# Performance work log

Measured on AMD Instinct MI355X. Metric: run time of the kernel, lower is better.

The kernel has to match this reference:

```python
import jax, jax.numpy as jnp
import numpy as np

B, N, D = 8, 4096, 64
NPOINT, NSAMPLE, RADIUS = 1024, 32, 0.2
MLP = [64, 64, 128]
IN_CH = 3 + D
EPS = 1e-5  # BatchNorm eps (torch default)


def setup_inputs() -> dict:
    key = jax.random.key(0)
    ks = jax.random.split(key, 2 + len(MLP))
    inp = {
        "xyz": jax.random.uniform(ks[0], (B, N, 3), jnp.float32),   # points in unit cube
        "points": jax.random.normal(ks[1], (B, N, D), jnp.float32),  # per-point features
    }
    last = IN_CH
    for i, out in enumerate(MLP):
        inp[f"w{i}"] = jax.random.normal(ks[2 + i], (out, last), jnp.float32) * 0.05  # 1x1 conv weight
        inp[f"b{i}"] = jnp.zeros((out,), jnp.float32)   # conv bias
        inp[f"g{i}"] = jnp.ones((out,), jnp.float32)    # BN gamma
        inp[f"be{i}"] = jnp.zeros((out,), jnp.float32)  # BN beta
        inp[f"m{i}"] = jnp.zeros((out,), jnp.float32)   # BN running mean
        inp[f"v{i}"] = jnp.ones((out,), jnp.float32)    # BN running var
        last = out
    return inp


def _fps(xyz, npoint):
    # Iterative farthest point sampling (deterministic start at index 0).
    Bb, Nn, _ = xyz.shape
    def step(carry, _):
        dist, far = carry
        centroid = xyz[jnp.arange(Bb), far][:, None, :]            # [B,1,3]
        d = jnp.sum((xyz - centroid) ** 2, axis=-1)                # [B,N]
        dist = jnp.minimum(dist, d)
        nfar = jnp.argmax(dist, axis=-1).astype(jnp.int32)
        return (dist, nfar), far
    init = (jnp.full((Bb, Nn), 1e10, xyz.dtype), jnp.zeros((Bb,), jnp.int32))
    _, idx = jax.lax.scan(step, init, None, length=npoint)
    return idx.T                                                   # [B,npoint]


def _index(p, idx):
    # p: [B,N,C], idx: [B,...] -> [B,...,C]
    return jax.vmap(lambda a, i: a[i])(p, idx)


def _ball_query(xyz, new_xyz):
    # For each query center, take first NSAMPLE point indices within RADIUS,
    # padding with the first found index (exactly PointNet++ query_ball_point).
    Nn = xyz.shape[1]
    sqr = jnp.sum((new_xyz[:, :, None, :] - xyz[:, None, :, :]) ** 2, axis=-1)  # [B,S,N]
    gidx = jnp.where(sqr > RADIUS ** 2, Nn, jnp.arange(Nn)[None, None, :])
    gidx = jnp.sort(gidx, axis=-1)[:, :, :NSAMPLE]                 # [B,S,K]
    first = gidx[:, :, :1]
    return jnp.where(gidx == Nn, first, gidx)


def reference(xyz, points, w0, b0, g0, be0, m0, v0,
              w1, b1, g1, be1, m1, v1,
              w2, b2, g2, be2, m2, v2):
    fps_idx = _fps(xyz, NPOINT)
    new_xyz = _index(xyz, fps_idx)                                 # [B,S,3]
    gidx = _ball_query(xyz, new_xyz)                               # [B,S,K]
    grouped_xyz = _index(xyz, gidx) - new_xyz[:, :, None, :]       # local coords [B,S,K,3]
    grouped_pts = _index(points, gidx)                             # [B,S,K,D]
    x = jnp.concatenate([grouped_xyz, grouped_pts], axis=-1)       # [B,S,K,3+D]
    layers = ((w0, b0, g0, be0, m0, v0),
              (w1, b1, g1, be1, m1, v1),
              (w2, b2, g2, be2, m2, v2))
    for w, b, g, be, m, v in layers:
        x = jnp.einsum('bskc,oc->bsko', x, w) + b                  # 1x1 conv (pointwise MLP)
        x = g * (x - m) * jax.lax.rsqrt(v + EPS) + be              # BN (eval mode)
        x = jax.nn.relu(x)
    new_points = jnp.max(x, axis=2)                                # max over neighbors -> [B,S,Cout]
    return new_xyz, new_points
```

## Files before the change

### kernel.cpp

```cpp
#include <hip/hip_runtime.h>
#include <hip/hip_bf16.h>
#include <stdint.h>

#define BATCH   8
#define NPTS    4096
#define DCH     64
#define NPOINT  1024
#define NSAMPLE 32
#define NEWXYZ_FLOATS (BATCH * NPOINT * 3)

typedef float v2f __attribute__((ext_vector_type(2)));

__device__ __forceinline__ float sqdist_rn(float px, float py, float pz,
                                           float cx, float cy, float cz) {
    float dx = __fsub_rn(px, cx);
    float dy = __fsub_rn(py, cy);
    float dz = __fsub_rn(pz, cz);
    return __fadd_rn(__fadd_rn(__fmul_rn(dx, dx), __fmul_rn(dy, dy)), __fmul_rn(dz, dz));
}

__device__ __forceinline__ unsigned long long ullmax(unsigned long long a, unsigned long long b) {
    return a > b ? a : b;
}

template <int CTRL>
__device__ __forceinline__ unsigned long long dpp_u64(unsigned long long v) {
    int lo = (int)(unsigned)(v & 0xFFFFFFFFull);
    int hi = (int)(unsigned)(v >> 32);
    lo = __builtin_amdgcn_update_dpp(0, lo, CTRL, 0xF, 0xF, true);
    hi = __builtin_amdgcn_update_dpp(0, hi, CTRL, 0xF, 0xF, true);
    return ((unsigned long long)(unsigned)hi << 32) | (unsigned)lo;
}

__global__ void prep_kernel(const float* __restrict__ w0, const float* __restrict__ b0,
                            const float* __restrict__ g0, const float* __restrict__ be0,
                            const float* __restrict__ m0, const float* __restrict__ v0,
                            const float* __restrict__ w1, const float* __restrict__ b1,
                            const float* __restrict__ g1, const float* __restrict__ be1,
                            const float* __restrict__ m1, const float* __restrict__ v1,
                            const float* __restrict__ w2, const float* __restrict__ b2,
                            const float* __restrict__ g2, const float* __restrict__ be2,
                            const float* __restrict__ m2, const float* __restrict__ v2,
                            float* __restrict__ wT0, float* __restrict__ wT1,
                            float* __restrict__ wT2, float* __restrict__ st) {
    const int tid  = blockIdx.x * blockDim.x + threadIdx.x;
    const int nthr = gridDim.x * blockDim.x;
    for (int i = tid; i < 64 * 67; i += nthr) {
        int o = i / 67, c = i % 67;
        wT0[c * 64 + (((o & 7) << 3) | (o >> 3))] = w0[i];
    }
    for (int i = tid; i < 64 * 64; i += nthr) {
        int o = i >> 6, c = i & 63;
        wT1[c * 64 + (((o & 7) << 3) | (o >> 3))] = w1[i];
    }
    for (int i = tid; i < 128 * 64; i += nthr) { int o = i >> 6, c = i & 63; wT2[c * 128 + o] = w2[i]; }
    if (tid < 64) {
        const int col = ((tid & 7) << 3) | (tid >> 3);
        float s = g0[tid] / sqrtf(v0[tid] + 1e-5f);
        st[col] = s;
        st[64 + col] = (b0[tid] - m0[tid]) * s + be0[tid];
        s = g1[tid] / sqrtf(v1[tid] + 1e-5f);
        st[128 + col] = s;
        st[192 + col] = (b1[tid] - m1[tid]) * s + be1[tid];
    }
    if (tid < 128) {
        float s = g2[tid] / sqrtf(v2[tid] + 1e-5f);
        st[256 + tid] = s;
        st[384 + tid] = (b2[tid] - m2[tid]) * s + be2[tid];
    }
}

__global__ __launch_bounds__(512, 1) void fps_kernel(const float* __restrict__ xyz,
                                                     float* __restrict__ newxyz) {
    __shared__ float4 sxyz[NPTS];
    __shared__ float4 snew[NPOINT];
    __shared__ unsigned long long kbuf[3];
    const int b    = blockIdx.x;
    const int tid  = threadIdx.x;
    const int lane = tid & 63;
    const float* xb = xyz + (size_t)b * NPTS * 3;

    v2f px[4], py[4], pz[4];
    float dd[8];
    unsigned invj[8];
#pragma unroll
    for (int i = 0; i < 8; ++i) {
        const int j = tid + i * 512;
        const float x = xb[3 * j], y = xb[3 * j + 1], z = xb[3 * j + 2];
        sxyz[j] = make_float4(x, y, z, 0.f);
        px[i >> 1][i & 1] = x;
        py[i >> 1][i & 1] = y;
        pz[i >> 1][i & 1] = z;
        dd[i] = 1e10f;
        invj[i] = 0xFFFFFFFFu - (unsigned)j;
    }
    if (tid < 3) kbuf[tid] = 0ull;

    float cx = xb[0], cy = xb[1], cz = xb[2];
    if (tid == 0) snew[0] = make_float4(cx, cy, cz, 0.f);
    __syncthreads();

    for (int t = 1; t < NPOINT; ++t) {
        const v2f ncx = {-cx, -cx}, ncy = {-cy, -cy}, ncz = {-cz, -cz};
#pragma unroll
        for (int k = 0; k < 4; ++k) {
            v2f dx, dy, dz, qx, qy, qz, s1, s2;
            asm("v_pk_add_f32 %0, %1, %2" : "=v"(dx) : "v"(px[k]), "v"(ncx));
            asm("v_pk_add_f32 %0, %1, %2" : "=v"(dy) : "v"(py[k]), "v"(ncy));
            asm("v_pk_add_f32 %0, %1, %2" : "=v"(dz) : "v"(pz[k]), "v"(ncz));
            asm("v_pk_mul_f32 %0, %1, %1" : "=v"(qx) : "v"(dx));
            asm("v_pk_mul_f32 %0, %1, %1" : "=v"(qy) : "v"(dy));
            asm("v_pk_mul_f32 %0, %1, %1" : "=v"(qz) : "v"(dz));
            asm("v_pk_add_f32 %0, %1, %2" : "=v"(s1) : "v"(qx), "v"(qy));
            asm("v_pk_add_f32 %0, %1, %2" : "=v"(s2) : "v"(s1), "v"(qz));
            dd[2 * k]     = fminf(dd[2 * k],     s2[0]);
            dd[2 * k + 1] = fminf(dd[2 * k + 1], s2[1]);
        }
        const float m = fmaxf(fmaxf(fmaxf(dd[0], dd[1]), fmaxf(dd[2], dd[3])),
                              fmaxf(fmaxf(dd[4], dd[5]), fmaxf(dd[6], dd[7])));
        unsigned inv = invj[0];
#pragma unroll
        for (int i = 7; i >= 0; --i)
            if (dd[i] == m) inv = invj[i];
        unsigned long long key =
            ((unsigned long long)__float_as_uint(m) << 32) | (unsigned long long)inv;
        key = ullmax(key, dpp_u64<0x111>(key));
        key = ullmax(key, dpp_u64<0x112>(key));
        key = ullmax(key, dpp_u64<0x114>(key));
        key = ullmax(key, dpp_u64<0x118>(key));
        key = ullmax(key, dpp_u64<0x142>(key));
        key = ullmax(key, dpp_u64<0x143>(key));
        if (lane == 63) atomicMax(&kbuf[t % 3], key);
        if (tid == 0) kbuf[(t + 1) % 3] = 0ull;
        __syncthreads();

        const unsigned long long v = kbuf[t % 3];
        const unsigned widx = 0xFFFFFFFFu - (unsigned)(v & 0xFFFFFFFFull);
        const float4 c = sxyz[widx];
        cx = c.x; cy = c.y; cz = c.z;
        if (tid == 0) snew[t] = make_float4(cx, cy, cz, 0.f);
    }
    __syncthreads();

    float* ob = newxyz + (size_t)b * NPOINT * 3;
    const float* sn = (const float*)snew;
#pragma unroll
    for (int k = tid; k < NPOINT * 3; k += 512) {
        const int p = k / 3, c = k - 3 * p;
        ob[k] = sn[4 * p + c];
    }
}

__global__ __launch_bounds__(256) void ballq_kernel(const float* __restrict__ xyz,
                                                    const float* __restrict__ newxyz,
                                                    int* __restrict__ gidx) {
    __shared__ int g[4][NSAMPLE];
    const int lane = threadIdx.x & 63;
    const int w    = threadIdx.x >> 6;
    const int q    = blockIdx.x * 4 + w;
    const int b    = q >> 10;
    const float* xb = xyz + (size_t)b * NPTS * 3;
    const float* c  = newxyz + (size_t)q * 3;
    const float cx = c[0], cy = c[1], cz = c[2];
    const float r2 = 0.04f;

    int cnt = 0;
    for (int base = 0; base < NPTS; base += 64) {
        const int j = base + lane;
        const float d = sqdist_rn(xb[j * 3 + 0], xb[j * 3 + 1], xb[j * 3 + 2], cx, cy, cz);
        const bool keep = !(d > r2);
        const unsigned long long m = __ballot(keep);
        if (keep) {
            const int slot = cnt + __popcll(m & ((1ull << lane) - 1ull));
            if (slot < NSAMPLE) g[w][slot] = j;
        }
        cnt += (int)__popcll(m);
        if (cnt >= NSAMPLE) break;
    }
    __syncthreads();
    const int first = g[w][0];
    if (lane < NSAMPLE) {
        const int v = (lane < cnt) ? g[w][lane] : first;
        gidx[(size_t)q * NSAMPLE + lane] = v;
    }
}

__global__ __launch_bounds__(256) void mlp_kernel(
    const float* __restrict__ xyz, const float* __restrict__ points,
    const float* __restrict__ newxyz, const int* __restrict__ gidx,
    const float* __restrict__ wT0, const float* __restrict__ wT1,
    const float* __restrict__ wT2, const float* __restrict__ st,
    float* __restrict__ outp) {
    __shared__ float Xs[4][68][36];
    const int lane = threadIdx.x & 63;
    const int w    = threadIdx.x >> 6;
    const int q    = blockIdx.x * 4 + w;
    const int b    = q >> 10;
    float (*X)[36] = Xs[w];
    const int* gi = gidx + (size_t)q * NSAMPLE;
    const float* nc = newxyz + (size_t)q * 3;
    const float c0 = nc[0], c1 = nc[1], c2 = nc[2];

    for (int k = 0; k < NSAMPLE; ++k) {
        const int idx = gi[k];
        X[3 + lane][k] = points[((size_t)b * NPTS + idx) * DCH + lane];
        if (lane < 3) {
            const float cv = (lane == 0) ? c0 : ((lane == 1) ? c1 : c2);
            X[lane][k] = xyz[((size_t)b * NPTS + idx) * 3 + lane] - cv;
        }
    }

    const int kk = lane >> 3;
    const int oo = lane & 7;

    float acc[4][8];
#pragma unroll
    for (int i = 0; i < 4; ++i)
#pragma unroll
        for (int j = 0; j < 8; ++j) acc[i][j] = 0.f;

    for (int c = 0; c < 67; ++c) {
        const float4 xv = *reinterpret_cast<const float4*>(&X[c][4 * kk]);
        const float4 wa = *reinterpret_cast<const float4*>(&wT0[c * 64 + 8 * oo]);
        const float4 wb = *reinterpret_cast<const float4*>(&wT0[c * 64 + 8 * oo + 4]);
        const float xr[4] = {xv.x, xv.y, xv.z, xv.w};
        const float wr[8] = {wa.x, wa.y, wa.z, wa.w, wb.x, wb.y, wb.z, wb.w};
#pragma unroll
        for (int i = 0; i < 4; ++i)
#pragma unroll
            for (int j = 0; j < 8; ++j)
                acc[i][j] = fmaf(xr[i], wr[j], acc[i][j]);
    }
    {
        const float4 sa = *reinterpret_cast<const float4*>(&st[8 * oo]);
        const float4 sb = *reinterpret_cast<const float4*>(&st[8 * oo + 4]);
        const float4 ta = *reinterpret_cast<const float4*>(&st[64 + 8 * oo]);
        const float4 tb = *reinterpret_cast<const float4*>(&st[64 + 8 * oo + 4]);
        const float sr[8] = {sa.x, sa.y, sa.z, sa.w, sb.x, sb.y, sb.z, sb.w};
        const float tr[8] = {ta.x, ta.y, ta.z, ta.w, tb.x, tb.y, tb.z, tb.w};
#pragma unroll
        for (int j = 0; j < 8; ++j) {
            float4 v;
            v.x = fmaxf(fmaf(acc[0][j], sr[j], tr[j]), 0.f);
            v.y = fmaxf(fmaf(acc[1][j], sr[j], tr[j]), 0.f);
            v.z = fmaxf(fmaf(acc[2][j], sr[j], tr[j]), 0.f);
            v.w = fmaxf(fmaf(acc[3][j], sr[j], tr[j]), 0.f);
            *reinterpret_cast<float4*>(&X[oo + 8 * j][4 * kk]) = v;
        }
    }

#pragma unroll
    for (int i = 0; i < 4; ++i)
#pragma unroll
        for (int j = 0; j < 8; ++j) acc[i][j] = 0.f;

    for (int c = 0; c < 64; ++c) {
        const float4 xv = *reinterpret_cast<const float4*>(&X[c][4 * kk]);
        const float4 wa = *reinterpret_cast<const float4*>(&wT1[c * 64 + 8 * oo]);
        const float4 wb = *reinterpret_cast<const float4*>(&wT1[c * 64 + 8 * oo + 4]);
        const float xr[4] = {xv.x, xv.y, xv.z, xv.w};
        const float wr[8] = {wa.x, wa.y, wa.z, wa.w, wb.x, wb.y, wb.z, wb.w};
#pragma unroll
        for (int i = 0; i < 4; ++i)
#pragma unroll
            for (int j = 0; j < 8; ++j)
                acc[i][j] = fmaf(xr[i], wr[j], acc[i][j]);
    }
    {
        const float4 sa = *reinterpret_cast<const float4*>(&st[128 + 8 * oo]);
        const float4 sb = *reinterpret_cast<const float4*>(&st[128 + 8 * oo + 4]);
        const float4 ta = *reinterpret_cast<const float4*>(&st[192 + 8 * oo]);
        const float4 tb = *reinterpret_cast<const float4*>(&st[192 + 8 * oo + 4]);
        const float sr[8] = {sa.x, sa.y, sa.z, sa.w, sb.x, sb.y, sb.z, sb.w};
        const float tr[8] = {ta.x, ta.y, ta.z, ta.w, tb.x, tb.y, tb.z, tb.w};
#pragma unroll
        for (int j = 0; j < 8; ++j) {
            float4 v;
            v.x = fmaxf(fmaf(acc[0][j], sr[j], tr[j]), 0.f);
            v.y = fmaxf(fmaf(acc[1][j], sr[j], tr[j]), 0.f);
            v.z = fmaxf(fmaf(acc[2][j], sr[j], tr[j]), 0.f);
            v.w = fmaxf(fmaf(acc[3][j], sr[j], tr[j]), 0.f);
            *reinterpret_cast<float4*>(&X[oo + 8 * j][4 * kk]) = v;
        }
    }

    float a2[4][16];
#pragma unroll
    for (int i = 0; i < 4; ++i)
#pragma unroll
        for (int j = 0; j < 16; ++j) a2[i][j] = 0.f;

    for (int c = 0; c < 64; ++c) {
        const float4 xv = *reinterpret_cast<const float4*>(&X[c][4 * kk]);
        const float xr[4] = {xv.x, xv.y, xv.z, xv.w};
        float wr[16];
#pragma unroll
        for (int j4 = 0; j4 < 4; ++j4) {
            const float4 wv = *reinterpret_cast<const float4*>(&wT2[c * 128 + 16 * oo + 4 * j4]);
            wr[4 * j4 + 0] = wv.x; wr[4 * j4 + 1] = wv.y;
            wr[4 * j4 + 2] = wv.z; wr[4 * j4 + 3] = wv.w;
        }
#pragma unroll
        for (int i = 0; i < 4; ++i)
#pragma unroll
            for (int j = 0; j < 16; ++j)
                a2[i][j] = fmaf(xr[i], wr[j], a2[i][j]);
    }

    float mx[16];
#pragma unroll
    for (int j = 0; j < 16; ++j) {
        const float sj = st[256 + 16 * oo + j];
        const float tj = st[384 + 16 * oo + j];
        float mm = fmaxf(fmaf(a2[0][j], sj, tj), 0.f);
        mm = fmaxf(mm, fmaxf(fmaf(a2[1][j], sj, tj), 0.f));
        mm = fmaxf(mm, fmaxf(fmaf(a2[2][j], sj, tj), 0.f));
        mm = fmaxf(mm, fmaxf(fmaf(a2[3][j], sj, tj), 0.f));
        mx[j] = mm;
    }
#pragma unroll
    for (int j = 0; j < 16; ++j) {
        mx[j] = fmaxf(mx[j], __shfl_xor(mx[j], 8, 64));
        mx[j] = fmaxf(mx[j], __shfl_xor(mx[j], 16, 64));
        mx[j] = fmaxf(mx[j], __shfl_xor(mx[j], 32, 64));
    }
    if (kk == 0) {
        float* dst = outp + (size_t)q * 128 + 16 * oo;
#pragma unroll
        for (int j4 = 0; j4 < 4; ++j4) {
            float4 v;
            v.x = mx[4 * j4 + 0]; v.y = mx[4 * j4 + 1];
            v.z = mx[4 * j4 + 2]; v.w = mx[4 * j4 + 3];
            *reinterpret_cast<float4*>(&dst[4 * j4]) = v;
        }
    }
}

extern "C" void kernel_launch(void* const* d_in, const int* in_sizes, int n_in,
                              void* d_out, int out_size, void* d_ws, size_t ws_size,
                              hipStream_t stream) {
    const float* xyz    = (const float*)d_in[0];
    const float* points = (const float*)d_in[1];
    const float* w0  = (const float*)d_in[2];
    const float* b0  = (const float*)d_in[3];
    const float* g0  = (const float*)d_in[4];
    const float* be0 = (const float*)d_in[5];
    const float* m0  = (const float*)d_in[6];
    const float* v0  = (const float*)d_in[7];
    const float* w1  = (const float*)d_in[8];
    const float* b1  = (const float*)d_in[9];
    const float* g1  = (const float*)d_in[10];
    const float* be1 = (const float*)d_in[11];
    const float* m1  = (const float*)d_in[12];
    const float* v1  = (const float*)d_in[13];
    const float* w2  = (const float*)d_in[14];
    const float* b2  = (const float*)d_in[15];
    const float* g2  = (const float*)d_in[16];
    const float* be2 = (const float*)d_in[17];
    const float* m2  = (const float*)d_in[18];
    const float* v2  = (const float*)d_in[19];

    float* out = (float*)d_out;
    float* ws  = (float*)d_ws;
    float* wT0 = ws;
    float* wT1 = ws + 4288;
    float* wT2 = ws + 8384;
    float* st  = ws + 16576;
    int*   gidx = (int*)(ws + 17088);

    prep_kernel<<<dim3(17), dim3(256), 0, stream>>>(w0, b0, g0, be0, m0, v0,
                                                    w1, b1, g1, be1, m1, v1,
                                                    w2, b2, g2, be2, m2, v2,
                                                    wT0, wT1, wT2, st);
    fps_kernel<<<dim3(BATCH), dim3(512), 0, stream>>>(xyz, out);
    ballq_kernel<<<dim3(2048), dim3(256), 0, stream>>>(xyz, out, gidx);
    mlp_kernel<<<dim3(2048), dim3(256), 0, stream>>>(xyz, points, out, gidx,
                                                     wT0, wT1, wT2, st,
                                                     out + NEWXYZ_FLOATS);
}
```

Before: 1.032 ms.

## Carry winner coordinates through FPS reduction and shrink block to four waves

The FPS kernel now uses 256 threads with 16 points each instead of 512 threads with 8. The argmax reduction carries the winning point's xyz alongside the key through the DPP steps. Each wave writes its key and coordinates to double-buffered shared slots, and every thread picks the winner from the four entries. This removes the shared atomicMax, the buffer reset and the dependent shared-memory lookup of the winner's coordinates, and halves the waves per barrier. The cost is more serial ALU work per thread, extra select chains and more register pressure.

Result: slower. 1.242 ms (+20.4%).

```diff
diff --git a/kernel.cpp b/kernel.cpp
--- a/kernel.cpp
+++ b/kernel.cpp
@@ -30,6 +30,25 @@
     lo = __builtin_amdgcn_update_dpp(0, lo, CTRL, 0xF, 0xF, true);
     hi = __builtin_amdgcn_update_dpp(0, hi, CTRL, 0xF, 0xF, true);
     return ((unsigned long long)(unsigned)hi << 32) | (unsigned)lo;
+}
+
+template <int CTRL>
+__device__ __forceinline__ float dpp_f32(float v) {
+    return __int_as_float(
+        __builtin_amdgcn_update_dpp(0, __float_as_int(v), CTRL, 0xF, 0xF, true));
+}
+
+template <int CTRL>
+__device__ __forceinline__ void red_step(unsigned long long& key, float& x, float& y, float& z) {
+    const unsigned long long ok = dpp_u64<CTRL>(key);
+    const float ox = dpp_f32<CTRL>(x);
+    const float oy = dpp_f32<CTRL>(y);
+    const float oz = dpp_f32<CTRL>(z);
+    const bool take = ok > key;
+    key = take ? ok : key;
+    x   = take ? ox : x;
+    y   = take ? oy : y;
+    z   = take ? oz : z;
 }
 
 __global__ void prep_kernel(const float* __restrict__ w0, const float* __restrict__ b0,
@@ -70,31 +89,27 @@
     }
 }
 
-__global__ __launch_bounds__(512, 1) void fps_kernel(const float* __restrict__ xyz,
+__global__ __launch_bounds__(256, 1) void fps_kernel(const float* __restrict__ xyz,
                                                      float* __restrict__ newxyz) {
-    __shared__ float4 sxyz[NPTS];
+    __shared__ __align__(16) unsigned long long skey[2][4];
+    __shared__ float4 scoord[2][4];
     __shared__ float4 snew[NPOINT];
-    __shared__ unsigned long long kbuf[3];
     const int b    = blockIdx.x;
     const int tid  = threadIdx.x;
     const int lane = tid & 63;
+    const int wid  = tid >> 6;
     const float* xb = xyz + (size_t)b * NPTS * 3;
 
-    v2f px[4], py[4], pz[4];
-    float dd[8];
-    unsigned invj[8];
-#pragma unroll
-    for (int i = 0; i < 8; ++i) {
-        const int j = tid + i * 512;
-        const float x = xb[3 * j], y = xb[3 * j + 1], z = xb[3 * j + 2];
-        sxyz[j] = make_float4(x, y, z, 0.f);
-        px[i >> 1][i & 1] = x;
-        py[i >> 1][i & 1] = y;
-        pz[i >> 1][i & 1] = z;
+    v2f px[8], py[8], pz[8];
+    float dd[16];
+#pragma unroll
+    for (int i = 0; i < 16; ++i) {
+        const int j = tid + i * 256;
+        px[i >> 1][i & 1] = xb[3 * j];
+        py[i >> 1][i & 1] = xb[3 * j + 1];
+        pz[i >> 1][i & 1] = xb[3 * j + 2];
         dd[i] = 1e10f;
-        invj[i] = 0xFFFFFFFFu - (unsigned)j;
-    }
-    if (tid < 3) kbuf[tid] = 0ull;
+    }
 
     float cx = xb[0], cy = xb[1], cz = xb[2];
     if (tid == 0) snew[0] = make_float4(cx, cy, cz, 0.f);
@@ -103,7 +118,7 @@
     for (int t = 1; t < NPOINT; ++t) {
         const v2f ncx = {-cx, -cx}, ncy = {-cy, -cy}, ncz = {-cz, -cz};
 #pragma unroll
-        for (int k = 0; k < 4; ++k) {
+        for (int k = 0; k < 8; ++k) {
             v2f dx, dy, dz, qx, qy, qz, s1, s2;
             asm("v_pk_add_f32 %0, %1, %2" : "=v"(dx) : "v"(px[k]), "v"(ncx));
             asm("v_pk_add_f32 %0, %1, %2" : "=v"(dy) : "v"(py[k]), "v"(ncy));
@@ -116,36 +131,62 @@
             dd[2 * k]     = fminf(dd[2 * k],     s2[0]);
             dd[2 * k + 1] = fminf(dd[2 * k + 1], s2[1]);
         }
-        const float m = fmaxf(fmaxf(fmaxf(dd[0], dd[1]), fmaxf(dd[2], dd[3])),
-                              fmaxf(fmaxf(dd[4], dd[5]), fmaxf(dd[6], dd[7])));
-        unsigned inv = invj[0];
-#pragma unroll
-        for (int i = 7; i >= 0; --i)
-            if (dd[i] == m) inv = invj[i];
+        float m = dd[0];
+#pragma unroll
+        for (int i = 1; i < 16; ++i) m = fmaxf(m, dd[i]);
+        int is = 15;
+#pragma unroll
+        for (int i = 14; i >= 0; --i)
+            if (dd[i] == m) is = i;
+        const unsigned inv = 0xFFFFFFFFu - (unsigned)(tid + (is << 8));
+        v2f a0 = (is & 8) ? px[4] : px[0], a1 = (is & 8) ? px[5] : px[1],
+            a2_ = (is & 8) ? px[6] : px[2], a3 = (is & 8) ? px[7] : px[3];
+        v2f b0 = (is & 8) ? py[4] : py[0], b1 = (is & 8) ? py[5] : py[1],
+            b2_ = (is & 8) ? py[6] : py[2], b3 = (is & 8) ? py[7] : py[3];
+        v2f g0 = (is & 8) ? pz[4] : pz[0], g1 = (is & 8) ? pz[5] : pz[1],
+            g2_ = (is & 8) ? pz[6] : pz[2], g3 = (is & 8) ? pz[7] : pz[3];
+        a0 = (is & 4) ? a2_ : a0; a1 = (is & 4) ? a3 : a1;
+        b0 = (is & 4) ? b2_ : b0; b1 = (is & 4) ? b3 : b1;
+        g0 = (is & 4) ? g2_ : g0; g1 = (is & 4) ? g3 : g1;
+        a0 = (is & 2) ? a1 : a0;
+        b0 = (is & 2) ? b1 : b0;
+        g0 = (is & 2) ? g1 : g0;
+        float wx = (is & 1) ? a0[1] : a0[0];
+        float wy = (is & 1) ? b0[1] : b0[0];
+        float wz = (is & 1) ? g0[1] : g0[0];
         unsigned long long key =
             ((unsigned long long)__float_as_uint(m) << 32) | (unsigned long long)inv;
-        key = ullmax(key, dpp_u64<0x111>(key));
-        key = ullmax(key, dpp_u64<0x112>(key));
-        key = ullmax(key, dpp_u64<0x114>(key));
-        key = ullmax(key, dpp_u64<0x118>(key));
-        key = ullmax(key, dpp_u64<0x142>(key));
-        key = ullmax(key, dpp_u64<0x143>(key));
-        if (lane == 63) atomicMax(&kbuf[t % 3], key);
-        if (tid == 0) kbuf[(t + 1) % 3] = 0ull;
+        red_step<0x111>(key, wx, wy, wz);
+        red_step<0x112>(key, wx, wy, wz);
+        red_step<0x114>(key, wx, wy, wz);
+        red_step<0x118>(key, wx, wy, wz);
+        red_step<0x142>(key, wx, wy, wz);
+        red_step<0x143>(key, wx, wy, wz);
+        if (lane == 63) {
+            skey[t & 1][wid]   = key;
+            scoord[t & 1][wid] = make_float4(wx, wy, wz, 0.f);
+        }
         __syncthreads();
 
-        const unsigned long long v = kbuf[t % 3];
-        const unsigned widx = 0xFFFFFFFFu - (unsigned)(v & 0xFFFFFFFFull);
-        const float4 c = sxyz[widx];
-        cx = c.x; cy = c.y; cz = c.z;
-        if (tid == 0) snew[t] = make_float4(cx, cy, cz, 0.f);
+        const ulonglong2* kp = (const ulonglong2*)(&skey[t & 1][0]);
+        const ulonglong2 ka = kp[0], kb = kp[1];
+        const float4 c0 = scoord[t & 1][0], c1 = scoord[t & 1][1];
+        const float4 c2 = scoord[t & 1][2], c3 = scoord[t & 1][3];
+        const bool t01 = ka.y > ka.x, t23 = kb.y > kb.x;
+        const unsigned long long k01 = t01 ? ka.y : ka.x;
+        const unsigned long long k23 = t23 ? kb.y : kb.x;
+        const float4 c01 = t01 ? c1 : c0;
+        const float4 c23 = t23 ? c3 : c2;
+        const bool tw = k23 > k01;
+        const float4 cw = tw ? c23 : c01;
+        cx = cw.x; cy = cw.y; cz = cw.z;
+        if (tid == 0) snew[t] = cw;
     }
     __syncthreads();
 
     float* ob = newxyz + (size_t)b * NPOINT * 3;
     const float* sn = (const float*)snew;
-#pragma unroll
-    for (int k = tid; k < NPOINT * 3; k += 512) {
+    for (int k = tid; k < NPOINT * 3; k += 256) {
         const int p = k / 3, c = k - 3 * p;
         ob[k] = sn[4 * p + c];
     }
@@ -372,7 +413,7 @@
                                                     w1, b1, g1, be1, m1, v1,
                                                     w2, b2, g2, be2, m2, v2,
                                                     wT0, wT1, wT2, st);
-    fps_kernel<<<dim3(BATCH), dim3(512), 0, stream>>>(xyz, out);
+    fps_kernel<<<dim3(BATCH), dim3(256), 0, stream>>>(xyz, out);
     ballq_kernel<<<dim3(2048), dim3(256), 0, stream>>>(xyz, out, gidx);
     mlp_kernel<<<dim3(2048), dim3(256), 0, stream>>>(xyz, points, out, gidx,
                                                      wT0, wT1, wT2, st,
```

## Run farthest point sampling with one wavefront per batch to drop block barriers

Applied to the files above, without the earlier changes.

The FPS kernel shrinks from 512 threads to a single 64-lane wavefront per batch, with each lane holding 64 points in registers. The per-iteration LDS atomicMax plus __syncthreads reduction is replaced by a DPP wave reduction and a readlane of the winning index. This removes the block-wide barrier and LDS round trip from each of the 1023 serial iterations. In exchange each lane does 8x more distance work per iteration, and the register arrays grow to about 256 VGPRs, which risks spills.

Result: slower. 1.990 ms (+92.8%).

```diff
diff --git a/kernel.cpp b/kernel.cpp
--- a/kernel.cpp
+++ b/kernel.cpp
@@ -70,40 +70,34 @@
     }
 }
 
-__global__ __launch_bounds__(512, 1) void fps_kernel(const float* __restrict__ xyz,
-                                                     float* __restrict__ newxyz) {
+__global__ __launch_bounds__(64, 1) void fps_kernel(const float* __restrict__ xyz,
+                                                    float* __restrict__ newxyz) {
     __shared__ float4 sxyz[NPTS];
     __shared__ float4 snew[NPOINT];
-    __shared__ unsigned long long kbuf[3];
     const int b    = blockIdx.x;
-    const int tid  = threadIdx.x;
-    const int lane = tid & 63;
+    const int lane = threadIdx.x;
     const float* xb = xyz + (size_t)b * NPTS * 3;
 
-    v2f px[4], py[4], pz[4];
-    float dd[8];
-    unsigned invj[8];
-#pragma unroll
-    for (int i = 0; i < 8; ++i) {
-        const int j = tid + i * 512;
+    v2f px[32], py[32], pz[32];
+    float dd[64];
+#pragma unroll
+    for (int i = 0; i < 64; ++i) {
+        const int j = i * 64 + lane;
         const float x = xb[3 * j], y = xb[3 * j + 1], z = xb[3 * j + 2];
         sxyz[j] = make_float4(x, y, z, 0.f);
         px[i >> 1][i & 1] = x;
         py[i >> 1][i & 1] = y;
         pz[i >> 1][i & 1] = z;
         dd[i] = 1e10f;
-        invj[i] = 0xFFFFFFFFu - (unsigned)j;
-    }
-    if (tid < 3) kbuf[tid] = 0ull;
-
+    }
     float cx = xb[0], cy = xb[1], cz = xb[2];
-    if (tid == 0) snew[0] = make_float4(cx, cy, cz, 0.f);
+    if (lane == 0) snew[0] = make_float4(cx, cy, cz, 0.f);
     __syncthreads();
 
     for (int t = 1; t < NPOINT; ++t) {
         const v2f ncx = {-cx, -cx}, ncy = {-cy, -cy}, ncz = {-cz, -cz};
 #pragma unroll
-        for (int k = 0; k < 4; ++k) {
+        for (int k = 0; k < 32; ++k) {
             v2f dx, dy, dz, qx, qy, qz, s1, s2;
             asm("v_pk_add_f32 %0, %1, %2" : "=v"(dx) : "v"(px[k]), "v"(ncx));
             asm("v_pk_add_f32 %0, %1, %2" : "=v"(dy) : "v"(py[k]), "v"(ncy));
@@ -116,12 +110,14 @@
             dd[2 * k]     = fminf(dd[2 * k],     s2[0]);
             dd[2 * k + 1] = fminf(dd[2 * k + 1], s2[1]);
         }
-        const float m = fmaxf(fmaxf(fmaxf(dd[0], dd[1]), fmaxf(dd[2], dd[3])),
-                              fmaxf(fmaxf(dd[4], dd[5]), fmaxf(dd[6], dd[7])));
-        unsigned inv = invj[0];
-#pragma unroll
-        for (int i = 7; i >= 0; --i)
-            if (dd[i] == m) inv = invj[i];
+        float m = dd[0];
+#pragma unroll
+        for (int i = 1; i < 64; ++i) m = fmaxf(m, dd[i]);
+        int is = 63;
+#pragma unroll
+        for (int i = 62; i >= 0; --i)
+            if (dd[i] == m) is = i;
+        const unsigned inv = 0xFFFFFFFFu - (unsigned)((is << 6) + lane);
         unsigned long long key =
             ((unsigned long long)__float_as_uint(m) << 32) | (unsigned long long)inv;
         key = ullmax(key, dpp_u64<0x111>(key));
@@ -130,22 +126,17 @@
         key = ullmax(key, dpp_u64<0x118>(key));
         key = ullmax(key, dpp_u64<0x142>(key));
         key = ullmax(key, dpp_u64<0x143>(key));
-        if (lane == 63) atomicMax(&kbuf[t % 3], key);
-        if (tid == 0) kbuf[(t + 1) % 3] = 0ull;
-        __syncthreads();
-
-        const unsigned long long v = kbuf[t % 3];
-        const unsigned widx = 0xFFFFFFFFu - (unsigned)(v & 0xFFFFFFFFull);
+        const unsigned lo63 = (unsigned)__builtin_amdgcn_readlane((int)(unsigned)(key & 0xFFFFFFFFull), 63);
+        const unsigned widx = 0xFFFFFFFFu - lo63;
         const float4 c = sxyz[widx];
         cx = c.x; cy = c.y; cz = c.z;
-        if (tid == 0) snew[t] = make_float4(cx, cy, cz, 0.f);
+        if (lane == 0) snew[t] = c;
     }
     __syncthreads();
 
     float* ob = newxyz + (size_t)b * NPOINT * 3;
     const float* sn = (const float*)snew;
-#pragma unroll
-    for (int k = tid; k < NPOINT * 3; k += 512) {
+    for (int k = lane; k < NPOINT * 3; k += 64) {
         const int p = k / 3, c = k - 3 * p;
         ob[k] = sn[4 * p + c];
     }
@@ -372,7 +363,7 @@
                                                     w1, b1, g1, be1, m1, v1,
                                                     w2, b2, g2, be2, m2, v2,
                                                     wT0, wT1, wT2, st);
-    fps_kernel<<<dim3(BATCH), dim3(512), 0, stream>>>(xyz, out);
+    fps_kernel<<<dim3(BATCH), dim3(64), 0, stream>>>(xyz, out);
     ballq_kernel<<<dim3(2048), dim3(256), 0, stream>>>(xyz, out, gidx);
     mlp_kernel<<<dim3(2048), dim3(256), 0, stream>>>(xyz, points, out, gidx,
                                                      wT0, wT1, wT2, st,
```
